# Performance work log

Measured on AMD Instinct MI355X. Metric: run time of the kernel, lower is better.

The kernel has to match this reference:

```python
import jax, jax.numpy as jnp
import numpy as np

B, M, F, U = 2048, 64, 512, 512  # batch, number_masks, num_features, units=ceil(F**1.0)

def setup_inputs() -> dict:
    key = jax.random.key(0)
    kx, kw = jax.random.split(key)
    x = jax.random.normal(kx, (B, M, F), dtype=jnp.float32)
    # glorot-uniform style init like keras Dense default
    limit = np.sqrt(6.0 / (F + U)).astype(np.float32)
    W = jax.random.uniform(kw, (M, F, U), dtype=jnp.float32, minval=-limit, maxval=limit)
    b = jnp.zeros((M, U), dtype=jnp.float32)
    return {"x": x, "W": W, "b": b}

def reference(x, W, b):
    # Per-mask Dense applied in a Python loop in the original == one batched GEMM.
    # y[b,m,u] = relu(sum_f x[b,m,f] * W[m,f,u] + b[m,u])
    y = jax.nn.relu(jnp.einsum('bmf,mfu->bmu', x, W) + b[None, :, :])
    # Concatenate along feature axis -> [B, M*U]
    return y.reshape(y.shape[0], -1)
```

## Files before the change

### kernel.cpp

```cpp
#include <hip/hip_runtime.h>
#include <hip/hip_bf16.h>


typedef __attribute__((ext_vector_type(8))) short bf16x8;
typedef __attribute__((ext_vector_type(4))) float f32x4;

#define LDS_S 40

__device__ __forceinline__ unsigned pk_bf16(float a, float b) {
    float2 t; t.x = a; t.y = b;
    __hip_bfloat162 h = __float22bfloat162_rn(t);
    union { __hip_bfloat162 h; unsigned u; } cv;
    cv.h = h;
    return cv.u;
}

__global__ void wt_prep_kernel(const float* __restrict__ W, short* __restrict__ Wt) {
    __shared__ float t[32][33];
    const int m  = blockIdx.z;
    const int f0 = blockIdx.y * 32;
    const int u0 = blockIdx.x * 32;
    const int tx = threadIdx.x;
    const int ty = threadIdx.y;
    const float* src = W + ((size_t)m * 512 + f0) * 512 + u0;
    #pragma unroll
    for (int i = 0; i < 4; ++i)
        t[ty + 8 * i][tx] = src[(size_t)(ty + 8 * i) * 512 + tx];
    __syncthreads();
    short* dst = Wt + ((size_t)m * 512 + u0) * 512 + f0;
    #pragma unroll
    for (int i = 0; i < 4; ++i) {
        float v = t[tx][ty + 8 * i];
        dst[(size_t)(ty + 8 * i) * 512 + tx] = (short)(pk_bf16(v, v) & 0xffff);
    }
}

__global__ __launch_bounds__(256) void pdense_main(const float* __restrict__ X,
                                                   const short* __restrict__ Wt,
                                                   const float* __restrict__ bias,
                                                   float* __restrict__ Out) {
    __shared__ short ldsA[2][128 * LDS_S];
    __shared__ short ldsB[2][128 * LDS_S];

    const int tid  = threadIdx.x;
    const int lane = tid & 63;
    const int wave = tid >> 6;
    const int q    = lane >> 4;
    const int ln   = lane & 15;
    const int wr   = (wave >> 1) * 64;
    const int wc   = (wave & 1) * 64;

    const int m    = blockIdx.y;
    const int ut   = blockIdx.x & 3;
    const int bt   = blockIdx.x >> 2;
    const int row0 = bt * 128;
    const int col0 = ut * 128;

    const int r0  = tid >> 2;
    const int k8  = (tid & 3) * 8;
    const int r1  = r0 + 64;
    const float* aP0 = X + (size_t)(row0 + r0) * 32768 + m * 512 + k8;
    const float* aP1 = X + (size_t)(row0 + r1) * 32768 + m * 512 + k8;
    const short* bP0 = Wt + (size_t)m * 262144 + (size_t)(col0 + r0) * 512 + k8;
    const short* bP1 = bP0 + 64 * 512;

    f32x4 acc[4][4];
    #pragma unroll
    for (int i = 0; i < 4; ++i)
        #pragma unroll
        for (int j = 0; j < 4; ++j)
            acc[i][j] = (f32x4)0.0f;

    float4 a_pre[4];
    uint4  b_pre[2];

    a_pre[0] = ((const float4*)aP0)[0];
    a_pre[1] = ((const float4*)aP0)[1];
    a_pre[2] = ((const float4*)aP1)[0];
    a_pre[3] = ((const float4*)aP1)[1];
    b_pre[0] = *(const uint4*)bP0;
    b_pre[1] = *(const uint4*)bP1;

    {
        uint4 w0, w1;
        w0.x = pk_bf16(a_pre[0].x, a_pre[0].y);
        w0.y = pk_bf16(a_pre[0].z, a_pre[0].w);
        w0.z = pk_bf16(a_pre[1].x, a_pre[1].y);
        w0.w = pk_bf16(a_pre[1].z, a_pre[1].w);
        *(uint4*)&ldsA[0][r0 * LDS_S + k8] = w0;
        w1.x = pk_bf16(a_pre[2].x, a_pre[2].y);
        w1.y = pk_bf16(a_pre[2].z, a_pre[2].w);
        w1.z = pk_bf16(a_pre[3].x, a_pre[3].y);
        w1.w = pk_bf16(a_pre[3].z, a_pre[3].w);
        *(uint4*)&ldsA[0][r1 * LDS_S + k8] = w1;
        *(uint4*)&ldsB[0][r0 * LDS_S + k8] = b_pre[0];
        *(uint4*)&ldsB[0][r1 * LDS_S + k8] = b_pre[1];
    }

    for (int kt = 0; kt < 16; ++kt) {
        const int p = kt & 1;
        __syncthreads();

        if (kt + 1 < 16) {
            const int ko = (kt + 1) * 32;
            a_pre[0] = ((const float4*)(aP0 + ko))[0];
            a_pre[1] = ((const float4*)(aP0 + ko))[1];
            a_pre[2] = ((const float4*)(aP1 + ko))[0];
            a_pre[3] = ((const float4*)(aP1 + ko))[1];
            b_pre[0] = *(const uint4*)(bP0 + ko);
            b_pre[1] = *(const uint4*)(bP1 + ko);
        }

        bf16x8 aF[4], bF[4];
        #pragma unroll
        for (int i = 0; i < 4; ++i)
            aF[i] = *(const bf16x8*)&ldsA[p][(wr + i * 16 + ln) * LDS_S + q * 8];
        #pragma unroll
        for (int j = 0; j < 4; ++j)
            bF[j] = *(const bf16x8*)&ldsB[p][(wc + j * 16 + ln) * LDS_S + q * 8];
        #pragma unroll
        for (int i = 0; i < 4; ++i)
            #pragma unroll
            for (int j = 0; j < 4; ++j)
                acc[i][j] = __builtin_amdgcn_mfma_f32_16x16x32_bf16(aF[i], bF[j], acc[i][j], 0, 0, 0);

        if (kt + 1 < 16) {
            const int pn = p ^ 1;
            uint4 w0, w1;
            w0.x = pk_bf16(a_pre[0].x, a_pre[0].y);
            w0.y = pk_bf16(a_pre[0].z, a_pre[0].w);
            w0.z = pk_bf16(a_pre[1].x, a_pre[1].y);
            w0.w = pk_bf16(a_pre[1].z, a_pre[1].w);
            *(uint4*)&ldsA[pn][r0 * LDS_S + k8] = w0;
            w1.x = pk_bf16(a_pre[2].x, a_pre[2].y);
            w1.y = pk_bf16(a_pre[2].z, a_pre[2].w);
            w1.z = pk_bf16(a_pre[3].x, a_pre[3].y);
            w1.w = pk_bf16(a_pre[3].z, a_pre[3].w);
            *(uint4*)&ldsA[pn][r1 * LDS_S + k8] = w1;
            *(uint4*)&ldsB[pn][r0 * LDS_S + k8] = b_pre[0];
            *(uint4*)&ldsB[pn][r1 * LDS_S + k8] = b_pre[1];
        }
    }

    #pragma unroll
    for (int j = 0; j < 4; ++j) {
        const int c = col0 + wc + j * 16 + ln;
        const float bv = bias[m * 512 + c];
        #pragma unroll
        for (int i = 0; i < 4; ++i) {
            const int r = row0 + wr + i * 16 + q * 4;
            float* op = Out + (size_t)r * 32768 + m * 512 + c;
            f32x4 v = acc[i][j];
            #pragma unroll
            for (int t = 0; t < 4; ++t) {
                float val = v[t] + bv;
                op[(size_t)t * 32768] = val > 0.0f ? val : 0.0f;
            }
        }
    }
}

__global__ void pdense_fallback(const float* __restrict__ X,
                                const float* __restrict__ Wp,
                                const float* __restrict__ bias,
                                float* __restrict__ Out) {
    __shared__ short ldsA[128 * LDS_S];
    __shared__ short ldsB[128 * LDS_S];

    const int tid  = threadIdx.x;
    const int lane = tid & 63;
    const int wave = tid >> 6;
    const int q    = lane >> 4;
    const int ln   = lane & 15;
    const int wr   = (wave >> 1) * 64;
    const int wc   = (wave & 1) * 64;

    const int m    = blockIdx.y;
    const int bt   = blockIdx.x & 15;
    const int ut   = blockIdx.x >> 4;
    const int row0 = bt * 128;
    const int col0 = ut * 128;

    const int ar0 = tid >> 2;
    const int ak0 = (tid & 3) * 8;
    const int ar1 = ar0 + 64;
    const float* aP0 = X + (size_t)(row0 + ar0) * 32768 + m * 512 + ak0;
    const float* aP1 = X + (size_t)(row0 + ar1) * 32768 + m * 512 + ak0;

    const int k0 = (tid & 7) * 4;
    const int u0 = (tid >> 3) * 4;
    const float* bP = Wp + (size_t)m * 262144 + (size_t)k0 * 512 + col0 + u0;

    f32x4 acc[4][4];
    #pragma unroll
    for (int i = 0; i < 4; ++i)
        #pragma unroll
        for (int j = 0; j < 4; ++j)
            acc[i][j] = (f32x4)0.0f;

    float4 a_pre[2][2];
    float4 b_pre[4];

    a_pre[0][0] = ((const float4*)aP0)[0];
    a_pre[0][1] = ((const float4*)aP0)[1];
    a_pre[1][0] = ((const float4*)aP1)[0];
    a_pre[1][1] = ((const float4*)aP1)[1];
    #pragma unroll
    for (int i = 0; i < 4; ++i)
        b_pre[i] = *(const float4*)(bP + (size_t)i * 512);

    for (int kt = 0; kt < 16; ++kt) {
        {
            uint4 w0, w1;
            w0.x = pk_bf16(a_pre[0][0].x, a_pre[0][0].y);
            w0.y = pk_bf16(a_pre[0][0].z, a_pre[0][0].w);
            w0.z = pk_bf16(a_pre[0][1].x, a_pre[0][1].y);
            w0.w = pk_bf16(a_pre[0][1].z, a_pre[0][1].w);
            *(uint4*)&ldsA[ar0 * LDS_S + ak0] = w0;
            w1.x = pk_bf16(a_pre[1][0].x, a_pre[1][0].y);
            w1.y = pk_bf16(a_pre[1][0].z, a_pre[1][0].w);
            w1.z = pk_bf16(a_pre[1][1].x, a_pre[1][1].y);
            w1.w = pk_bf16(a_pre[1][1].z, a_pre[1][1].w);
            *(uint4*)&ldsA[ar1 * LDS_S + ak0] = w1;
            #pragma unroll
            for (int j = 0; j < 4; ++j) {
                float c0 = ((const float*)&b_pre[0])[j];
                float c1 = ((const float*)&b_pre[1])[j];
                float c2 = ((const float*)&b_pre[2])[j];
                float c3 = ((const float*)&b_pre[3])[j];
                uint2 wv;
                wv.x = pk_bf16(c0, c1);
                wv.y = pk_bf16(c2, c3);
                *(uint2*)&ldsB[(u0 + j) * LDS_S + k0] = wv;
            }
        }
        __syncthreads();

        if (kt + 1 < 16) {
            const int ko = (kt + 1) * 32;
            a_pre[0][0] = ((const float4*)(aP0 + ko))[0];
            a_pre[0][1] = ((const float4*)(aP0 + ko))[1];
            a_pre[1][0] = ((const float4*)(aP1 + ko))[0];
            a_pre[1][1] = ((const float4*)(aP1 + ko))[1];
            #pragma unroll
            for (int i = 0; i < 4; ++i)
                b_pre[i] = *(const float4*)(bP + (size_t)(ko + i) * 512);
        }

        bf16x8 aF[4], bF[4];
        #pragma unroll
        for (int i = 0; i < 4; ++i)
            aF[i] = *(const bf16x8*)&ldsA[(wr + i * 16 + ln) * LDS_S + q * 8];
        #pragma unroll
        for (int j = 0; j < 4; ++j)
            bF[j] = *(const bf16x8*)&ldsB[(wc + j * 16 + ln) * LDS_S + q * 8];
        #pragma unroll
        for (int i = 0; i < 4; ++i)
            #pragma unroll
            for (int j = 0; j < 4; ++j)
                acc[i][j] = __builtin_amdgcn_mfma_f32_16x16x32_bf16(aF[i], bF[j], acc[i][j], 0, 0, 0);

        __syncthreads();
    }

    #pragma unroll
    for (int j = 0; j < 4; ++j) {
        const int c = col0 + wc + j * 16 + ln;
        const float bv = bias[m * 512 + c];
        #pragma unroll
        for (int i = 0; i < 4; ++i) {
            const int r = row0 + wr + i * 16 + q * 4;
            float* op = Out + (size_t)r * 32768 + m * 512 + c;
            f32x4 v = acc[i][j];
            #pragma unroll
            for (int t = 0; t < 4; ++t) {
                float val = v[t] + bv;
                op[(size_t)t * 32768] = val > 0.0f ? val : 0.0f;
            }
        }
    }
}

extern "C" void kernel_launch(void* const* d_in, const int* in_sizes, int n_in,
                              void* d_out, int out_size, void* d_ws, size_t ws_size,
                              hipStream_t stream) {
    const float* x    = (const float*)d_in[0];
    const float* W    = (const float*)d_in[1];
    const float* bias = (const float*)d_in[2];
    float* out = (float*)d_out;

    const size_t wt_bytes = (size_t)64 * 512 * 512 * sizeof(short);
    if (ws_size >= wt_bytes) {
        short* Wt = (short*)d_ws;
        hipLaunchKernelGGL(wt_prep_kernel, dim3(16, 16, 64), dim3(32, 8), 0, stream, W, Wt);
        hipLaunchKernelGGL(pdense_main, dim3(64, 64), dim3(256), 0, stream, x, Wt, bias, out);
    } else {
        hipLaunchKernelGGL(pdense_fallback, dim3(64, 64), dim3(256), 0, stream, W ? x : x, W, bias, out);
    }
}
```

Measured before the change: 612.3 us.

## Stream X and Wt tiles directly to LDS with swizzle and XCD-aware block mapping

The register-staged prefetch plus convert-and-store path is replaced by direct global-to-LDS loads (global_load_lds, 16 bytes) for both the fp32 X tile and the bf16 Wt tile. Both tiles use an XOR swizzle instead of padding, and the fp32-to-bf16 conversion of X moves to the fragment-read stage. The grid is flattened and remapped so that all blocks for a given mask land on the same XCD, which is meant to improve L2 reuse of Wt and X. The A tile now occupies twice the LDS because it is stored as fp32, and conversion now happens per fragment read, so the converted values are not shared across waves.

```diff
diff --git a/kernel.cpp b/kernel.cpp
--- a/kernel.cpp
+++ b/kernel.cpp
@@ -13,6 +13,12 @@
     union { __hip_bfloat162 h; unsigned u; } cv;
     cv.h = h;
     return cv.u;
+}
+
+__device__ __forceinline__ void gld16(const void* g, void* l) {
+    __builtin_amdgcn_global_load_lds(
+        (const __attribute__((address_space(1))) void*)g,
+        (__attribute__((address_space(3))) void*)l, 16, 0, 0);
 }
 
 __global__ void wt_prep_kernel(const float* __restrict__ W, short* __restrict__ Wt) {
@@ -35,12 +41,12 @@
     }
 }
 
-__global__ __launch_bounds__(256) void pdense_main(const float* __restrict__ X,
-                                                   const short* __restrict__ Wt,
-                                                   const float* __restrict__ bias,
-                                                   float* __restrict__ Out) {
-    __shared__ short ldsA[2][128 * LDS_S];
-    __shared__ short ldsB[2][128 * LDS_S];
+__global__ __launch_bounds__(256, 3) void pdense_main(const float* __restrict__ X,
+                                                      const short* __restrict__ Wt,
+                                                      const float* __restrict__ bias,
+                                                      float* __restrict__ Out) {
+    __shared__ float ldsA[2][128 * 32];
+    __shared__ short ldsB[2][128 * 32];
 
     const int tid  = threadIdx.x;
     const int lane = tid & 63;
@@ -50,19 +56,22 @@
     const int wr   = (wave >> 1) * 64;
     const int wc   = (wave & 1) * 64;
 
-    const int m    = blockIdx.y;
-    const int ut   = blockIdx.x & 3;
-    const int bt   = blockIdx.x >> 2;
+    const int id   = blockIdx.x;
+    const int xcd  = id & 7;
+    const int slot = id >> 3;
+    const int m    = xcd * 8 + (slot >> 6);
+    const int rem  = slot & 63;
+    const int bt   = rem >> 2;
+    const int ut   = rem & 3;
     const int row0 = bt * 128;
     const int col0 = ut * 128;
 
-    const int r0  = tid >> 2;
-    const int k8  = (tid & 3) * 8;
-    const int r1  = r0 + 64;
-    const float* aP0 = X + (size_t)(row0 + r0) * 32768 + m * 512 + k8;
-    const float* aP1 = X + (size_t)(row0 + r1) * 32768 + m * 512 + k8;
-    const short* bP0 = Wt + (size_t)m * 262144 + (size_t)(col0 + r0) * 512 + k8;
-    const short* bP1 = bP0 + 64 * 512;
+    const int arow = wave * 32 + (lane >> 3);
+    const int ac   = (lane & 7) ^ (lane >> 3);
+    const float* agp = X + (size_t)(row0 + arow) * 32768 + m * 512 + ac * 4;
+    const int brow = wave * 32 + (lane >> 2);
+    const int bc   = (lane & 3) ^ ((lane >> 3) & 3);
+    const short* bgp = Wt + (size_t)m * 262144 + (size_t)(col0 + brow) * 512 + bc * 8;
 
     f32x4 acc[4][4];
     #pragma unroll
@@ -71,31 +80,15 @@
         for (int j = 0; j < 4; ++j)
             acc[i][j] = (f32x4)0.0f;
 
-    float4 a_pre[4];
-    uint4  b_pre[2];
-
-    a_pre[0] = ((const float4*)aP0)[0];
-    a_pre[1] = ((const float4*)aP0)[1];
-    a_pre[2] = ((const float4*)aP1)[0];
-    a_pre[3] = ((const float4*)aP1)[1];
-    b_pre[0] = *(const uint4*)bP0;
-    b_pre[1] = *(const uint4*)bP1;
-
-    {
-        uint4 w0, w1;
-        w0.x = pk_bf16(a_pre[0].x, a_pre[0].y);
-        w0.y = pk_bf16(a_pre[0].z, a_pre[0].w);
-        w0.z = pk_bf16(a_pre[1].x, a_pre[1].y);
-        w0.w = pk_bf16(a_pre[1].z, a_pre[1].w);
-        *(uint4*)&ldsA[0][r0 * LDS_S + k8] = w0;
-        w1.x = pk_bf16(a_pre[2].x, a_pre[2].y);
-        w1.y = pk_bf16(a_pre[2].z, a_pre[2].w);
-        w1.z = pk_bf16(a_pre[3].x, a_pre[3].y);
-        w1.w = pk_bf16(a_pre[3].z, a_pre[3].w);
-        *(uint4*)&ldsA[0][r1 * LDS_S + k8] = w1;
-        *(uint4*)&ldsB[0][r0 * LDS_S + k8] = b_pre[0];
-        *(uint4*)&ldsB[0][r1 * LDS_S + k8] = b_pre[1];
-    }
+    #pragma unroll
+    for (int i = 0; i < 4; ++i)
+        gld16(agp + (size_t)i * 8 * 32768, &ldsA[0][(wave * 32 + i * 8) * 32]);
+    #pragma unroll
+    for (int j = 0; j < 2; ++j)
+        gld16(bgp + (size_t)j * 16 * 512, &ldsB[0][(wave * 32 + j * 16) * 32]);
+
+    const int s1 = (ln >> 1) & 3;
+    const int s0 = ln & 1;
 
     for (int kt = 0; kt < 16; ++kt) {
         const int p = kt & 1;
@@ -103,43 +96,38 @@
 
         if (kt + 1 < 16) {
             const int ko = (kt + 1) * 32;
-            a_pre[0] = ((const float4*)(aP0 + ko))[0];
-            a_pre[1] = ((const float4*)(aP0 + ko))[1];
-            a_pre[2] = ((const float4*)(aP1 + ko))[0];
-            a_pre[3] = ((const float4*)(aP1 + ko))[1];
-            b_pre[0] = *(const uint4*)(bP0 + ko);
-            b_pre[1] = *(const uint4*)(bP1 + ko);
+            #pragma unroll
+            for (int i = 0; i < 4; ++i)
+                gld16(agp + ko + (size_t)i * 8 * 32768, &ldsA[p ^ 1][(wave * 32 + i * 8) * 32]);
+            #pragma unroll
+            for (int j = 0; j < 2; ++j)
+                gld16(bgp + ko + (size_t)j * 16 * 512, &ldsB[p ^ 1][(wave * 32 + j * 16) * 32]);
         }
 
         bf16x8 aF[4], bF[4];
         #pragma unroll
-        for (int i = 0; i < 4; ++i)
-            aF[i] = *(const bf16x8*)&ldsA[p][(wr + i * 16 + ln) * LDS_S + q * 8];
-        #pragma unroll
-        for (int j = 0; j < 4; ++j)
-            bF[j] = *(const bf16x8*)&ldsB[p][(wc + j * 16 + ln) * LDS_S + q * 8];
+        for (int i = 0; i < 4; ++i) {
+            const int r = wr + i * 16 + ln;
+            const float* base = &ldsA[p][r * 32 + ((q ^ s1) << 3)];
+            float4 ca = *(const float4*)(base + (s0 << 2));
+            float4 cb = *(const float4*)(base + ((1 - s0) << 2));
+            union { bf16x8 v; uint4 u; } fr;
+            fr.u.x = pk_bf16(ca.x, ca.y);
+            fr.u.y = pk_bf16(ca.z, ca.w);
+            fr.u.z = pk_bf16(cb.x, cb.y);
+            fr.u.w = pk_bf16(cb.z, cb.w);
+            aF[i] = fr.v;
+        }
+        #pragma unroll
+        for (int j = 0; j < 4; ++j) {
+            const int r = wc + j * 16 + ln;
+            bF[j] = *(const bf16x8*)&ldsB[p][r * 32 + ((q ^ s1) << 3)];
+        }
         #pragma unroll
         for (int i = 0; i < 4; ++i)
             #pragma unroll
             for (int j = 0; j < 4; ++j)
                 acc[i][j] = __builtin_amdgcn_mfma_f32_16x16x32_bf16(aF[i], bF[j], acc[i][j], 0, 0, 0);
-
-        if (kt + 1 < 16) {
-            const int pn = p ^ 1;
-            uint4 w0, w1;
-            w0.x = pk_bf16(a_pre[0].x, a_pre[0].y);
-            w0.y = pk_bf16(a_pre[0].z, a_pre[0].w);
-            w0.z = pk_bf16(a_pre[1].x, a_pre[1].y);
-            w0.w = pk_bf16(a_pre[1].z, a_pre[1].w);
-            *(uint4*)&ldsA[pn][r0 * LDS_S + k8] = w0;
-            w1.x = pk_bf16(a_pre[2].x, a_pre[2].y);
-            w1.y = pk_bf16(a_pre[2].z, a_pre[2].w);
-            w1.z = pk_bf16(a_pre[3].x, a_pre[3].y);
-            w1.w = pk_bf16(a_pre[3].z, a_pre[3].w);
-            *(uint4*)&ldsA[pn][r1 * LDS_S + k8] = w1;
-            *(uint4*)&ldsB[pn][r0 * LDS_S + k8] = b_pre[0];
-            *(uint4*)&ldsB[pn][r1 * LDS_S + k8] = b_pre[1];
-        }
     }
 
     #pragma unroll
@@ -293,8 +281,8 @@
     if (ws_size >= wt_bytes) {
         short* Wt = (short*)d_ws;
         hipLaunchKernelGGL(wt_prep_kernel, dim3(16, 16, 64), dim3(32, 8), 0, stream, W, Wt);
-        hipLaunchKernelGGL(pdense_main, dim3(64, 64), dim3(256), 0, stream, x, Wt, bias, out);
+        hipLaunchKernelGGL(pdense_main, dim3(4096), dim3(256), 0, stream, x, Wt, bias, out);
     } else {
-        hipLaunchKernelGGL(pdense_fallback, dim3(64, 64), dim3(256), 0, stream, W ? x : x, W, bias, out);
-    }
-}
+        hipLaunchKernelGGL(pdense_fallback, dim3(64, 64), dim3(256), 0, stream, x, W, bias, out);
+    }
+}
```

After: 597.5 us. 2.4% less time.
